# Performance work log

Hardware: AMD Instinct MI355X
Metric: run time of the kernel (lower is better)

The kernel has to match this reference:

```python
import jax, jax.numpy as jnp
import numpy as np

B, T, D, H = 4, 4096, 1280, 5120  # batch, tokens (64x64 SAM grid), embedding_dim, mlp_dim


def setup_inputs() -> dict:
    key = jax.random.key(0)
    k = jax.random.split(key, 5)
    # int8 quantized activations and weights (symmetric, per-tensor)
    x = jax.random.randint(k[0], (B, T, D), -128, 128, dtype=jnp.int8)
    w1 = jax.random.randint(k[1], (H, D), -128, 128, dtype=jnp.int8)  # lin1.weight [out,in]
    b1 = jax.random.normal(k[2], (H,), jnp.float32) * 0.02            # fp32 bias
    w2 = jax.random.randint(k[3], (D, H), -128, 128, dtype=jnp.int8)  # lin2.weight [out,in]
    b2 = jax.random.normal(k[4], (D,), jnp.float32) * 0.02
    a1 = jnp.float32(0.05 * 0.01)   # input_scale * w1_scale (dequant alpha of lin1)
    s_req = jnp.float32(0.08)       # lin2_input_scale (requant scale after GELU)
    a2 = jnp.float32(0.08 * 0.01)   # lin2_input_scale * w2_scale (dequant alpha of lin2)
    return dict(x=x, w1=w1, b1=b1, w2=w2, b2=b2, a1=a1, s_req=s_req, a2=a2)


def reference(x, w1, b1, w2, b2, a1, s_req, a2):
    acc1 = jnp.einsum('btd,hd->bth', x.astype(jnp.int32), w1.astype(jnp.int32))
    h = acc1.astype(jnp.float32) * a1 + b1              # [B,T,H] fp32
    # exact (erf) GELU, then requantize to int8 for lin2's input
    g = jax.nn.gelu(h, approximate=False)
    q = jnp.clip(jnp.round(g / s_req), -128, 127).astype(jnp.int8)
    acc2 = jnp.einsum('bth,dh->btd', q.astype(jnp.int32), w2.astype(jnp.int32))
    return acc2.astype(jnp.float32) * a2 + b2           # [B,T,D] fp32
```

## Files before the change

kernel.cpp:

```cpp
#include <hip/hip_runtime.h>
#include <stdint.h>
#include <math.h>

typedef __attribute__((ext_vector_type(4))) int i32x4;
typedef __attribute__((ext_vector_type(16))) int i32x16;
typedef __attribute__((ext_vector_type(4))) float f32x4;

constexpr int D_DIM = 1280;
constexpr int H_DIM = 5120;

__device__ __forceinline__ void gload_lds16(const void* g, void* l) {
  __builtin_amdgcn_global_load_lds(
      (const __attribute__((address_space(1))) void*)g,
      (__attribute__((address_space(3))) void*)l,
      16, 0, 0);
}

__global__ void __launch_bounds__(256) k_packw(const int* __restrict__ s1,
                                               const int* __restrict__ s2,
                                               int8_t* __restrict__ out,
                                               long wn) {
  long i = ((long)blockIdx.x * 256 + threadIdx.x) * 16;
  const int* p = (i < wn) ? (s1 + i) : (s2 + (i - wn));
  i32x4 a = *(const i32x4*)(p);
  i32x4 b = *(const i32x4*)(p + 4);
  i32x4 c = *(const i32x4*)(p + 8);
  i32x4 d = *(const i32x4*)(p + 12);
  i32x4 r;
  r.x = (a.x & 255) | ((a.y & 255) << 8) | ((a.z & 255) << 16) | (a.w << 24);
  r.y = (b.x & 255) | ((b.y & 255) << 8) | ((b.z & 255) << 16) | (b.w << 24);
  r.z = (c.x & 255) | ((c.y & 255) << 8) | ((c.z & 255) << 16) | (c.w << 24);
  r.w = (d.x & 255) | ((d.y & 255) << 8) | ((d.z & 255) << 16) | (d.w << 24);
  *(i32x4*)(out + i) = r;
}

__global__ void __launch_bounds__(256) k_pack(const int* __restrict__ in,
                                              int8_t* __restrict__ out,
                                              long n) {
  long i = ((long)blockIdx.x * 256 + threadIdx.x) * 16;
  if (i >= n) return;
  const int* p = in + i;
  i32x4 a = *(const i32x4*)(p);
  i32x4 b = *(const i32x4*)(p + 4);
  i32x4 c = *(const i32x4*)(p + 8);
  i32x4 d = *(const i32x4*)(p + 12);
  i32x4 r;
  r.x = (a.x & 255) | ((a.y & 255) << 8) | ((a.z & 255) << 16) | (a.w << 24);
  r.y = (b.x & 255) | ((b.y & 255) << 8) | ((b.z & 255) << 16) | (b.w << 24);
  r.z = (c.x & 255) | ((c.y & 255) << 8) | ((c.z & 255) << 16) | (c.w << 24);
  r.w = (d.x & 255) | ((d.y & 255) << 8) | ((d.z & 255) << 16) | (d.w << 24);
  *(i32x4*)(out + i) = r;
}

template <int KDIM, int ODIM, bool GELU, bool GROUP_C>
__global__ void __launch_bounds__(256, 2)
k_gemm(const int8_t* __restrict__ P, const int8_t* __restrict__ S,
       const float* __restrict__ bias, const float* __restrict__ ps1,
       const float* __restrict__ ps2, void* __restrict__ Cout,
       int rtiles, int ctiles) {
  constexpr int BKB = 64;
  constexpr int NT = KDIM / BKB;
  __shared__ __align__(16) int8_t smem[49152];

  const int nwg = rtiles * ctiles;
  int rt, ct;
  {
    const int bid = blockIdx.x;
    const int q = nwg >> 3, r = nwg & 7, x = bid & 7, l = bid >> 3;
    const int swz = (x < r ? x * (q + 1) : r * (q + 1) + (x - r) * q) + l;
    if (GROUP_C && (ctiles & 3) == 0) {
      const int G = rtiles * 4, g = swz / G, rr = swz % G;
      rt = rr >> 2; ct = g * 4 + (rr & 3);
    } else if (!GROUP_C && (rtiles & 3) == 0) {
      const int G = ctiles * 4, g = swz / G, rr = swz % G;
      ct = rr >> 2; rt = g * 4 + (rr & 3);
    } else {
      rt = swz / ctiles; ct = swz % ctiles;
    }
  }

  const int tid = threadIdx.x;
  const int lane = tid & 63, wid = tid >> 6;
  const int wr = wid >> 1, wc = wid & 1;
  const int r32 = lane & 31, hi5 = lane >> 5;

  const int srow = tid >> 2;
  const int ssl  = ((tid & 3) ^ (srow & 3)) << 4;
  const int8_t* Pth = P + (size_t)(rt * 256 + srow) * KDIM + ssl;
  const int8_t* Sth = S + (size_t)(ct * 128 + srow) * KDIM + ssl;
  const int dT = tid * 16;

  auto STAGE = [&](int buf, int t) {
    const int8_t* ga = Pth + t * BKB;
    const int8_t* gb = Sth + t * BKB;
#pragma unroll
    for (int p = 0; p < 4; ++p)
      gload_lds16(ga + (size_t)(p * 64) * KDIM, smem + buf * 16384 + p * 4096 + dT);
#pragma unroll
    for (int p = 0; p < 2; ++p)
      gload_lds16(gb + (size_t)(p * 64) * KDIM,
                  smem + 32768 + buf * 8192 + p * 4096 + dT);
  };

  const int ksl = r32 & 3;
  const int ko0 = ((0 + hi5) ^ ksl) << 4;
  const int ko1 = ((2 + hi5) ^ ksl) << 4;
  const int rowA = (wr * 128 + r32) * 64;
  const int rowB = (wc * 64 + r32) * 64;

  i32x16 acc[4][2] = {};

  auto COMPUTE = [&](int buf) {
    const int8_t* Ab = smem + buf * 16384;
    const int8_t* Bb = smem + 32768 + buf * 8192;
#pragma unroll
    for (int ks = 0; ks < 2; ++ks) {
      const int ko = ks ? ko1 : ko0;
      i32x4 pf[4], sf[2];
#pragma unroll
      for (int i = 0; i < 4; ++i) pf[i] = *(const i32x4*)(Ab + rowA + i * 2048 + ko);
#pragma unroll
      for (int j = 0; j < 2; ++j) sf[j] = *(const i32x4*)(Bb + rowB + j * 2048 + ko);
      __builtin_amdgcn_s_setprio(1);
#pragma unroll
      for (int i = 0; i < 4; ++i)
#pragma unroll
        for (int j = 0; j < 2; ++j)
          acc[i][j] =
              __builtin_amdgcn_mfma_i32_32x32x32_i8(pf[i], sf[j], acc[i][j], 0, 0, 0);
      __builtin_amdgcn_s_setprio(0);
    }
  };

  STAGE(0, 0);
  __syncthreads();
#pragma unroll 1
  for (int t = 0; t < NT; t += 2) {
    STAGE(1, t + 1);
    COMPUTE(0);
    __syncthreads();
    if (t + 2 < NT) STAGE(0, t + 2);
    COMPUTE(1);
    __syncthreads();
  }

  const float s1 = *ps1;
  if constexpr (GELU) {
    const float rs = 1.0f / (*ps2);
    int8_t* Q = (int8_t*)Cout;
    int8_t* lb = smem;
#pragma unroll
    for (int i = 0; i < 4; ++i) {
#pragma unroll
      for (int qq = 0; qq < 4; ++qq) {
        const int hb = wr * 128 + i * 32 + qq * 8 + hi5 * 4;
        const f32x4 bv = *(const f32x4*)(bias + rt * 256 + hb);
#pragma unroll
        for (int j = 0; j < 2; ++j) {
          const int tok = wc * 64 + j * 32 + r32;
          uint32_t pk = 0;
#pragma unroll
          for (int rr = 0; rr < 4; ++rr) {
            const float h = __builtin_fmaf((float)acc[i][j][qq * 4 + rr], s1, bv[rr]);
            const float e = __expf(-1.702f * h);
            const float g = h * __builtin_amdgcn_rcpf(1.0f + e);
            float qf = rintf(g * rs);
            qf = fminf(127.0f, fmaxf(-128.0f, qf));
            pk |= ((uint32_t)((int)qf & 255)) << (rr * 8);
          }
          const int sl = (hb >> 4) ^ (tok & 7) ^ ((tok & 24) >> 1);
          *(uint32_t*)(lb + tok * 256 + (sl << 4) + (hb & 12)) = pk;
        }
      }
    }
    __syncthreads();
#pragma unroll
    for (int it = 0; it < 8; ++it) {
      const int row = it * 16 + (tid >> 4);
      const int sl = tid & 15;
      const int s2 = sl ^ (row & 7) ^ ((row & 24) >> 1);
      i32x4 v = *(const i32x4*)(lb + row * 256 + (s2 << 4));
      *(i32x4*)(Q + (size_t)(ct * 128 + row) * ODIM + rt * 256 + sl * 16) = v;
    }
  } else {
    float* O = (float*)Cout;
#pragma unroll
    for (int i = 0; i < 4; ++i) {
#pragma unroll
      for (int j = 0; j < 2; ++j) {
        const int col = ct * 128 + wc * 64 + j * 32 + r32;
        const float bv = bias[col];
#pragma unroll
        for (int qq = 0; qq < 4; ++qq)
#pragma unroll
          for (int rr = 0; rr < 4; ++rr) {
            const int row = rt * 256 + wr * 128 + i * 32 + qq * 8 + hi5 * 4 + rr;
            O[(size_t)row * ODIM + col] =
                __builtin_fmaf((float)acc[i][j][qq * 4 + rr], s1, bv);
          }
      }
    }
  }
}

extern "C" void kernel_launch(void* const* d_in, const int* in_sizes, int n_in,
                              void* d_out, int out_size, void* d_ws, size_t ws_size,
                              hipStream_t stream) {
  (void)in_sizes; (void)n_in; (void)out_size;
  const int*   x32  = (const int*)d_in[0];
  const int*   w132 = (const int*)d_in[1];
  const float* b1   = (const float*)d_in[2];
  const int*   w232 = (const int*)d_in[3];
  const float* b2   = (const float*)d_in[4];
  const float* a1   = (const float*)d_in[5];
  const float* sreq = (const float*)d_in[6];
  const float* a2   = (const float*)d_in[7];
  float* out = (float*)d_out;

  const int M = 4 * 4096;
  const size_t WN = (size_t)H_DIM * D_DIM;

  int8_t* w1p  = (int8_t*)d_ws;
  int8_t* w2p  = w1p + WN;
  int8_t* base = w2p + WN;

  size_t avail = ws_size > 2 * WN ? ws_size - 2 * WN : 0;
  size_t rows = avail / (size_t)(D_DIM + H_DIM);
  int Mc = (int)((rows / 1024) * 1024);
  if (Mc < 1024) Mc = (int)((rows / 256) * 256);
  if (Mc < 256) Mc = 256;
  if (Mc > M) Mc = M;

  k_packw<<<(int)(2 * WN / 4096), 256, 0, stream>>>(w132, w232, w1p, (long)WN);

  for (int m0 = 0; m0 < M; m0 += Mc) {
    const int mc = (M - m0 < Mc) ? (M - m0) : Mc;
    int8_t* xp = base;
    int8_t* q  = base + (size_t)Mc * D_DIM;
    const size_t nx = (size_t)mc * D_DIM;
    k_pack<<<(int)(nx / 4096), 256, 0, stream>>>(x32 + (size_t)m0 * D_DIM, xp, (long)nx);
    k_gemm<D_DIM, H_DIM, true, true><<<20 * (mc / 128), 256, 0, stream>>>(
        w1p, xp, b1, a1, sreq, q, 20, mc / 128);
    k_gemm<H_DIM, D_DIM, false, false><<<(mc / 256) * 10, 256, 0, stream>>>(
        q, w2p, b2, a2, nullptr, out + (size_t)m0 * D_DIM, mc / 256, 10);
  }
}
```

Baseline: 319.8 us.

## Fuse weight and activation packing, retune LDS swizzles, use nontemporal output stores

Merges the weight-pack and activation-pack kernels into one launch when the whole batch fits in workspace, saving a kernel launch. It changes the LDS XOR swizzle for the GEMM operand tiles to key on row pairs, and replaces the swizzled GELU staging buffer with a padded 260-byte row stride read back as scalar ints. It also switches the fp32 output stores of the second GEMM to nontemporal stores to avoid polluting cache. The new swizzle and padding may change bank-conflict behaviour, and the scalar LDS reads add instructions.

```diff
diff --git a/kernel.cpp b/kernel.cpp
--- a/kernel.cpp
+++ b/kernel.cpp
@@ -16,12 +16,7 @@
       16, 0, 0);
 }
 
-__global__ void __launch_bounds__(256) k_packw(const int* __restrict__ s1,
-                                               const int* __restrict__ s2,
-                                               int8_t* __restrict__ out,
-                                               long wn) {
-  long i = ((long)blockIdx.x * 256 + threadIdx.x) * 16;
-  const int* p = (i < wn) ? (s1 + i) : (s2 + (i - wn));
+__device__ __forceinline__ i32x4 pack16(const int* __restrict__ p) {
   i32x4 a = *(const i32x4*)(p);
   i32x4 b = *(const i32x4*)(p + 4);
   i32x4 c = *(const i32x4*)(p + 8);
@@ -31,7 +26,19 @@
   r.y = (b.x & 255) | ((b.y & 255) << 8) | ((b.z & 255) << 16) | (b.w << 24);
   r.z = (c.x & 255) | ((c.y & 255) << 8) | ((c.z & 255) << 16) | (c.w << 24);
   r.w = (d.x & 255) | ((d.y & 255) << 8) | ((d.z & 255) << 16) | (d.w << 24);
-  *(i32x4*)(out + i) = r;
+  return r;
+}
+
+__global__ void __launch_bounds__(256) k_pack3(const int* __restrict__ s1,
+                                               const int* __restrict__ s2,
+                                               const int* __restrict__ s3,
+                                               int8_t* __restrict__ out,
+                                               long wn, long nx) {
+  long i = ((long)blockIdx.x * 256 + threadIdx.x) * 16;
+  if (i >= 2 * wn + nx) return;
+  const int* p = (i < wn) ? (s1 + i)
+               : (i < 2 * wn) ? (s2 + (i - wn)) : (s3 + (i - 2 * wn));
+  *(i32x4*)(out + i) = pack16(p);
 }
 
 __global__ void __launch_bounds__(256) k_pack(const int* __restrict__ in,
@@ -39,17 +46,7 @@
                                               long n) {
   long i = ((long)blockIdx.x * 256 + threadIdx.x) * 16;
   if (i >= n) return;
-  const int* p = in + i;
-  i32x4 a = *(const i32x4*)(p);
-  i32x4 b = *(const i32x4*)(p + 4);
-  i32x4 c = *(const i32x4*)(p + 8);
-  i32x4 d = *(const i32x4*)(p + 12);
-  i32x4 r;
-  r.x = (a.x & 255) | ((a.y & 255) << 8) | ((a.z & 255) << 16) | (a.w << 24);
-  r.y = (b.x & 255) | ((b.y & 255) << 8) | ((b.z & 255) << 16) | (b.w << 24);
-  r.z = (c.x & 255) | ((c.y & 255) << 8) | ((c.z & 255) << 16) | (c.w << 24);
-  r.w = (d.x & 255) | ((d.y & 255) << 8) | ((d.z & 255) << 16) | (d.w << 24);
-  *(i32x4*)(out + i) = r;
+  *(i32x4*)(out + i) = pack16(in + i);
 }
 
 template <int KDIM, int ODIM, bool GELU, bool GROUP_C>
@@ -85,42 +82,42 @@
   const int r32 = lane & 31, hi5 = lane >> 5;
 
   const int srow = tid >> 2;
-  const int ssl  = ((tid & 3) ^ (srow & 3)) << 4;
+  const int ssl  = (((tid & 3) ^ ((srow >> 1) & 3)) << 4);
   const int8_t* Pth = P + (size_t)(rt * 256 + srow) * KDIM + ssl;
   const int8_t* Sth = S + (size_t)(ct * 128 + srow) * KDIM + ssl;
   const int dT = tid * 16;
 
   auto STAGE = [&](int buf, int t) {
-    const int8_t* ga = Pth + t * BKB;
-    const int8_t* gb = Sth + t * BKB;
+    const int8_t* gp = Pth + t * BKB;
+    const int8_t* gs = Sth + t * BKB;
 #pragma unroll
     for (int p = 0; p < 4; ++p)
-      gload_lds16(ga + (size_t)(p * 64) * KDIM, smem + buf * 16384 + p * 4096 + dT);
+      gload_lds16(gp + (size_t)(p * 64) * KDIM, smem + buf * 16384 + p * 4096 + dT);
 #pragma unroll
     for (int p = 0; p < 2; ++p)
-      gload_lds16(gb + (size_t)(p * 64) * KDIM,
+      gload_lds16(gs + (size_t)(p * 64) * KDIM,
                   smem + 32768 + buf * 8192 + p * 4096 + dT);
   };
 
-  const int ksl = r32 & 3;
-  const int ko0 = ((0 + hi5) ^ ksl) << 4;
-  const int ko1 = ((2 + hi5) ^ ksl) << 4;
-  const int rowA = (wr * 128 + r32) * 64;
-  const int rowB = (wc * 64 + r32) * 64;
+  const int sw2 = (r32 >> 1) & 3;
+  const int ko0 = ((0 + hi5) ^ sw2) << 4;
+  const int ko1 = ((2 + hi5) ^ sw2) << 4;
+  const int rowP = (wr * 128 + r32) * 64;
+  const int rowS = (wc * 64 + r32) * 64;
 
   i32x16 acc[4][2] = {};
 
   auto COMPUTE = [&](int buf) {
-    const int8_t* Ab = smem + buf * 16384;
-    const int8_t* Bb = smem + 32768 + buf * 8192;
+    const int8_t* Pb = smem + buf * 16384 + rowP;
+    const int8_t* Sb = smem + 32768 + buf * 8192 + rowS;
 #pragma unroll
     for (int ks = 0; ks < 2; ++ks) {
       const int ko = ks ? ko1 : ko0;
       i32x4 pf[4], sf[2];
 #pragma unroll
-      for (int i = 0; i < 4; ++i) pf[i] = *(const i32x4*)(Ab + rowA + i * 2048 + ko);
-#pragma unroll
-      for (int j = 0; j < 2; ++j) sf[j] = *(const i32x4*)(Bb + rowB + j * 2048 + ko);
+      for (int i = 0; i < 4; ++i) pf[i] = *(const i32x4*)(Pb + i * 2048 + ko);
+#pragma unroll
+      for (int j = 0; j < 2; ++j) sf[j] = *(const i32x4*)(Sb + j * 2048 + ko);
       __builtin_amdgcn_s_setprio(1);
 #pragma unroll
       for (int i = 0; i < 4; ++i)
@@ -153,8 +150,8 @@
     for (int i = 0; i < 4; ++i) {
 #pragma unroll
       for (int qq = 0; qq < 4; ++qq) {
-        const int hb = wr * 128 + i * 32 + qq * 8 + hi5 * 4;
-        const f32x4 bv = *(const f32x4*)(bias + rt * 256 + hb);
+        const int hl = wr * 128 + i * 32 + qq * 8 + hi5 * 4;
+        const f32x4 bv = *(const f32x4*)(bias + rt * 256 + hl);
 #pragma unroll
         for (int j = 0; j < 2; ++j) {
           const int tok = wc * 64 + j * 32 + r32;
@@ -168,8 +165,7 @@
             qf = fminf(127.0f, fmaxf(-128.0f, qf));
             pk |= ((uint32_t)((int)qf & 255)) << (rr * 8);
           }
-          const int sl = (hb >> 4) ^ (tok & 7) ^ ((tok & 24) >> 1);
-          *(uint32_t*)(lb + tok * 256 + (sl << 4) + (hb & 12)) = pk;
+          *(uint32_t*)(lb + tok * 260 + hl) = pk;
         }
       }
     }
@@ -178,8 +174,12 @@
     for (int it = 0; it < 8; ++it) {
       const int row = it * 16 + (tid >> 4);
       const int sl = tid & 15;
-      const int s2 = sl ^ (row & 7) ^ ((row & 24) >> 1);
-      i32x4 v = *(const i32x4*)(lb + row * 256 + (s2 << 4));
+      const int8_t* rp = lb + row * 260 + sl * 16;
+      i32x4 v;
+      v.x = *(const int*)(rp);
+      v.y = *(const int*)(rp + 4);
+      v.z = *(const int*)(rp + 8);
+      v.w = *(const int*)(rp + 12);
       *(i32x4*)(Q + (size_t)(ct * 128 + row) * ODIM + rt * 256 + sl * 16) = v;
     }
   } else {
@@ -195,8 +195,9 @@
 #pragma unroll
           for (int rr = 0; rr < 4; ++rr) {
             const int row = rt * 256 + wr * 128 + i * 32 + qq * 8 + hi5 * 4 + rr;
-            O[(size_t)row * ODIM + col] =
-                __builtin_fmaf((float)acc[i][j][qq * 4 + rr], s1, bv);
+            __builtin_nontemporal_store(
+                __builtin_fmaf((float)acc[i][j][qq * 4 + rr], s1, bv),
+                &O[(size_t)row * ODIM + col]);
           }
       }
     }
@@ -231,8 +232,22 @@
   if (Mc < 256) Mc = 256;
   if (Mc > M) Mc = M;
 
-  k_packw<<<(int)(2 * WN / 4096), 256, 0, stream>>>(w132, w232, w1p, (long)WN);
-
+  if (Mc == M) {
+    const long nx = (long)M * D_DIM;
+    const long tot = 2 * (long)WN + nx;
+    int8_t* xp = base;
+    int8_t* q  = base + (size_t)M * D_DIM;
+    k_pack3<<<(int)(tot / 4096), 256, 0, stream>>>(w132, w232, x32, w1p,
+                                                   (long)WN, nx);
+    k_gemm<D_DIM, H_DIM, true, true><<<20 * (M / 128), 256, 0, stream>>>(
+        w1p, xp, b1, a1, sreq, q, 20, M / 128);
+    k_gemm<H_DIM, D_DIM, false, false><<<(M / 256) * 10, 256, 0, stream>>>(
+        q, w2p, b2, a2, nullptr, out, M / 256, 10);
+    return;
+  }
+
+  k_pack3<<<(int)(2 * WN / 4096), 256, 0, stream>>>(w132, w232, x32, w1p,
+                                                    (long)WN, 0);
   for (int m0 = 0; m0 < M; m0 += Mc) {
     const int mc = (M - m0 < Mc) ? (M - m0) : Mc;
     int8_t* xp = base;
```

After: 292.5 us. 8.6% less time.
